# Kernel tuning notes

Measured on AMD Instinct MI355X. Metric: run time of the kernel, lower is better.

The kernel has to match this reference:

```python
import jax, jax.numpy as jnp
import numpy as np

EPS = 1e-5

def ln(x, g, b):
    m = x.mean(-1, keepdims=True)
    v = x.var(-1, keepdims=True)
    return (x - m) / jnp.sqrt(v + EPS) * g + b

def setup_inputs() -> dict:
    key = jax.random.key(0)
    ks = jax.random.split(key, 16)
    def p(k, shape, fan):
        return jax.random.normal(k, shape, jnp.float32) * (1.0 / np.sqrt(fan))
    B, N, M = 4, 256, 256
    C = 256
    inp = {}
    inp["tracks"] = jax.random.normal(ks[0], (B, 1028, N), jnp.float32)
    inp["detections"] = jax.random.normal(ks[1], (B, 1028, M), jnp.float32)
    # app encoder: Linear(1024,256) -> LN -> ReLU -> Linear(256,256)
    inp["wa1"] = p(ks[2], (1024, C), 1024); inp["ba1"] = jnp.zeros((C,), jnp.float32)
    inp["gla"] = jnp.ones((C,), jnp.float32); inp["bla"] = jnp.zeros((C,), jnp.float32)
    inp["wa2"] = p(ks[3], (C, C), C); inp["ba2"] = jnp.zeros((C,), jnp.float32)
    # geo encoder: Linear(4,128) -> LN -> ReLU -> Linear(128,256)
    inp["wg1"] = p(ks[4], (4, C // 2), 4); inp["bg1"] = jnp.zeros((C // 2,), jnp.float32)
    inp["glg"] = jnp.ones((C // 2,), jnp.float32); inp["blg"] = jnp.zeros((C // 2,), jnp.float32)
    inp["wg2"] = p(ks[5], (C // 2, C), C // 2); inp["bg2"] = jnp.zeros((C,), jnp.float32)
    # fusion LayerNorm
    inp["gf"] = jnp.ones((C,), jnp.float32); inp["bf"] = jnp.zeros((C,), jnp.float32)
    # cross-attention (4 heads, head_dim 64)
    inp["wq"] = p(ks[6], (C, C), C); inp["bq"] = jnp.zeros((C,), jnp.float32)
    inp["wk"] = p(ks[7], (C, C), C); inp["bk"] = jnp.zeros((C,), jnp.float32)
    inp["wv"] = p(ks[8], (C, C), C); inp["bv"] = jnp.zeros((C,), jnp.float32)
    inp["wo"] = p(ks[9], (C, C), C); inp["bo"] = jnp.zeros((C,), jnp.float32)
    # classifier: Linear(512,128) -> ReLU -> Linear(128,1)
    inp["wc1"] = p(ks[10], (2 * C, 128), 2 * C); inp["bc1"] = jnp.zeros((128,), jnp.float32)
    inp["wc2"] = p(ks[11], (128, 1), 128); inp["bc2"] = jnp.zeros((1,), jnp.float32)
    return inp

def reference(tracks, detections, wa1, ba1, gla, bla, wa2, ba2,
              wg1, bg1, glg, blg, wg2, bg2, gf, bf,
              wq, bq, wk, bk, wv, bv, wo, bo,
              wc1, bc1, wc2, bc2):
    tr = tracks.transpose(0, 2, 1)       # (B, N, 1028)
    de = detections.transpose(0, 2, 1)   # (B, M, 1028)

    def encode(x):
        app, geo = x[..., :1024], x[..., 1024:]
        h = jax.nn.relu(ln(app @ wa1 + ba1, gla, bla)) @ wa2 + ba2
        g = jax.nn.relu(ln(geo @ wg1 + bg1, glg, blg)) @ wg2 + bg2
        return ln(h + g, gf, bf)

    t_emb = encode(tr)   # (B, N, C)
    d_emb = encode(de)   # (B, M, C)

    B, N, C = t_emb.shape
    M = d_emb.shape[1]
    H, dh = 4, C // 4

    # Cross-attention (computed in the original forward but its output is never used)
    q = (t_emb @ wq + bq).reshape(B, N, H, dh)
    k = (d_emb @ wk + bk).reshape(B, M, H, dh)
    v = (d_emb @ wv + bv).reshape(B, M, H, dh)
    att = jax.nn.softmax(jnp.einsum('bnhd,bmhd->bhnm', q, k) / jnp.sqrt(jnp.float32(dh)), axis=-1)
    attn_out = jnp.einsum('bhnm,bmhd->bnhd', att, v).reshape(B, N, C) @ wo + bo  # unused, as in original

    # Pairwise classifier. cat([t_rep, d_rep], -1) @ wc1 == t @ wc1[:C] + d @ wc1[C:]
    a = t_emb @ wc1[:C]   # (B, N, 128)
    c = d_emb @ wc1[C:]   # (B, M, 128)
    h = jax.nn.relu(a[:, :, None, :] + c[:, None, :, :] + bc1)  # (B, N, M, 128)
    logits = (h @ wc2 + bc2)[..., 0]  # (B, N, M)
    return logits
```

## Files before the change

kernel.cpp:

```cpp
#include <hip/hip_runtime.h>

#define EPS 1e-5f


__global__ __launch_bounds__(256, 2) void k_gemm1(
    const float* __restrict__ tracks, const float* __restrict__ dets,
    const float* __restrict__ wa1, float* __restrict__ part)
{
    __shared__ __align__(16) float xs[128 * 32];
    const int blk = blockIdx.x;
    const int rt  = blk >> 3;
    const int ksi = blk & 7;
    const int g0  = rt * 32;
    const int side = g0 >> 10, b = (g0 >> 8) & 3, n0 = g0 & 255;
    const float* xb = (side ? dets : tracks) + (size_t)b * (1028 * 256);
    const int k0 = ksi * 128;
    const int tid = threadIdx.x;
    const int w   = tid >> 6;
    const int c0  = (tid & 63) * 4;

    for (int t = tid; t < 1024; t += 256) {
        int f = t >> 3, r4 = (t & 7) << 2;
        *(float4*)(xs + f * 32 + r4) =
            *(const float4*)(xb + (size_t)(k0 + f) * 256 + n0 + r4);
    }
    __syncthreads();

    float acc[8][4];
#pragma unroll
    for (int i = 0; i < 8; ++i)
#pragma unroll
        for (int j = 0; j < 4; ++j) acc[i][j] = 0.f;

    const float* wptr = wa1 + (size_t)k0 * 256 + c0;
    float4 wb[2][8];
#pragma unroll
    for (int j = 0; j < 8; ++j)
        wb[0][j] = *(const float4*)(wptr + (size_t)j * 256);

#pragma unroll
    for (int bb = 0; bb < 16; ++bb) {
        const int cur = bb & 1, nxt = cur ^ 1;
        if (bb < 15) {
#pragma unroll
            for (int j = 0; j < 8; ++j)
                wb[nxt][j] =
                    *(const float4*)(wptr + (size_t)((bb + 1) * 8 + j) * 256);
        }
#pragma unroll
        for (int j = 0; j < 8; ++j) {
            const int f = bb * 8 + j;
            float4 x0 = *(const float4*)(xs + f * 32 + w * 8);
            float4 x1 = *(const float4*)(xs + f * 32 + w * 8 + 4);
            float4 wv = wb[cur][j];
            float xv[8] = {x0.x, x0.y, x0.z, x0.w, x1.x, x1.y, x1.z, x1.w};
#pragma unroll
            for (int i = 0; i < 8; ++i) {
                acc[i][0] = fmaf(xv[i], wv.x, acc[i][0]);
                acc[i][1] = fmaf(xv[i], wv.y, acc[i][1]);
                acc[i][2] = fmaf(xv[i], wv.z, acc[i][2]);
                acc[i][3] = fmaf(xv[i], wv.w, acc[i][3]);
            }
        }
    }
    float* pb = part + ((size_t)ksi * 2048 + g0 + w * 8) * 256 + c0;
#pragma unroll
    for (int i = 0; i < 8; ++i)
        *(float4*)(pb + (size_t)i * 256) =
            make_float4(acc[i][0], acc[i][1], acc[i][2], acc[i][3]);
}

__global__ __launch_bounds__(256, 2) void k_tail(
    const float* __restrict__ tracks, const float* __restrict__ dets,
    const float* __restrict__ part,
    const float* __restrict__ ba1, const float* __restrict__ gla,
    const float* __restrict__ bla,
    const float* __restrict__ wg1, const float* __restrict__ bg1,
    const float* __restrict__ glg, const float* __restrict__ blg,
    const float* __restrict__ wa2, const float* __restrict__ ba2,
    const float* __restrict__ wg2, const float* __restrict__ bg2,
    const float* __restrict__ gf,  const float* __restrict__ bf,
    const float* __restrict__ wc1,
    float* __restrict__ aout, float* __restrict__ cout)
{
    __shared__ __align__(16) float h1e[384 * 4];
    __shared__ __align__(16) float psum[16 * 256];
    __shared__ __align__(16) float emb[256 * 4];
    __shared__ float ps2[2][4][128];
    __shared__ float red[4][4][2];
    __shared__ float geo_s[4][4];

    const int blk = blockIdx.x;
    const int g0 = blk * 4;
    const int side = g0 >> 10, b = (g0 >> 8) & 3, n0 = g0 & 255;
    const float* xb = (side ? dets : tracks) + (size_t)b * (1028 * 256);
    const int tid = threadIdx.x, w = tid >> 6, lane = tid & 63, c = tid;

    if (tid < 16)
        geo_s[tid >> 2][tid & 3] =
            xb[(size_t)(1024 + (tid & 3)) * 256 + n0 + (tid >> 2)];

    float h[4];
#pragma unroll
    for (int i = 0; i < 4; ++i) {
        float s = ba1[c];
#pragma unroll
        for (int s8 = 0; s8 < 8; ++s8)
            s += part[((size_t)s8 * 2048 + g0 + i) * 256 + c];
        h[i] = s;
    }
#pragma unroll
    for (int i = 0; i < 4; ++i) {
        float s = h[i], s2 = h[i] * h[i];
#pragma unroll
        for (int off = 32; off >= 1; off >>= 1) {
            s  += __shfl_xor(s,  off, 64);
            s2 += __shfl_xor(s2, off, 64);
        }
        if (lane == 0) { red[w][i][0] = s; red[w][i][1] = s2; }
    }
    __syncthreads();
    {
        float gv = gla[c], bv = bla[c];
#pragma unroll
        for (int i = 0; i < 4; ++i) {
            float s  = red[0][i][0] + red[1][i][0] + red[2][i][0] + red[3][i][0];
            float s2 = red[0][i][1] + red[1][i][1] + red[2][i][1] + red[3][i][1];
            float m   = s * (1.f / 256.f);
            float var = s2 * (1.f / 256.f) - m * m;
            h1e[c * 4 + i] =
                fmaxf((h[i] - m) * rsqrtf(var + EPS) * gv + bv, 0.f);
        }
    }
    __syncthreads();

    float gh[4];
    if (tid < 128) {
        const int j = tid;
#pragma unroll
        for (int i = 0; i < 4; ++i) {
            float s = bg1[j];
#pragma unroll
            for (int f = 0; f < 4; ++f)
                s = fmaf(geo_s[i][f], wg1[f * 128 + j], s);
            gh[i] = s;
        }
#pragma unroll
        for (int i = 0; i < 4; ++i) {
            float s = gh[i], s2 = gh[i] * gh[i];
#pragma unroll
            for (int off = 32; off >= 1; off >>= 1) {
                s  += __shfl_xor(s,  off, 64);
                s2 += __shfl_xor(s2, off, 64);
            }
            if (lane == 0) { red[w][i][0] = s; red[w][i][1] = s2; }
        }
    }
    __syncthreads();
    if (tid < 128) {
        const int j = tid;
        float gv = glg[j], bv = blg[j];
#pragma unroll
        for (int i = 0; i < 4; ++i) {
            float s  = red[0][i][0] + red[1][i][0];
            float s2 = red[0][i][1] + red[1][i][1];
            float m   = s * (1.f / 128.f);
            float var = s2 * (1.f / 128.f) - m * m;
            h1e[(256 + j) * 4 + i] =
                fmaxf((gh[i] - m) * rsqrtf(var + EPS) * gv + bv, 0.f);
        }
    }
    __syncthreads();

    const int c0 = lane * 4;
    float acc[4][4];
#pragma unroll
    for (int i = 0; i < 4; ++i)
#pragma unroll
        for (int j = 0; j < 4; ++j) acc[i][j] = 0.f;

    {
        const int ka = w * 64;
#pragma unroll 4
        for (int k = 0; k < 64; ++k) {
            float4 xv = *(const float4*)(h1e + (ka + k) * 4);
            float4 wv = *(const float4*)(wa2 + (size_t)(ka + k) * 256 + c0);
#pragma unroll
            for (int i = 0; i < 4; ++i) {
                float x = (&xv.x)[i];
                acc[i][0] = fmaf(x, wv.x, acc[i][0]);
                acc[i][1] = fmaf(x, wv.y, acc[i][1]);
                acc[i][2] = fmaf(x, wv.z, acc[i][2]);
                acc[i][3] = fmaf(x, wv.w, acc[i][3]);
            }
        }
        const int kg = w * 32;
#pragma unroll 4
        for (int k = 0; k < 32; ++k) {
            float4 xv = *(const float4*)(h1e + (256 + kg + k) * 4);
            float4 wv = *(const float4*)(wg2 + (size_t)(kg + k) * 256 + c0);
#pragma unroll
            for (int i = 0; i < 4; ++i) {
                float x = (&xv.x)[i];
                acc[i][0] = fmaf(x, wv.x, acc[i][0]);
                acc[i][1] = fmaf(x, wv.y, acc[i][1]);
                acc[i][2] = fmaf(x, wv.z, acc[i][2]);
                acc[i][3] = fmaf(x, wv.w, acc[i][3]);
            }
        }
    }
#pragma unroll
    for (int i = 0; i < 4; ++i)
        *(float4*)(psum + (w * 4 + i) * 256 + c0) =
            make_float4(acc[i][0], acc[i][1], acc[i][2], acc[i][3]);
    __syncthreads();

    float h2[4];
#pragma unroll
    for (int i = 0; i < 4; ++i) {
        float s = ba2[c] + bg2[c];
#pragma unroll
        for (int w4 = 0; w4 < 4; ++w4)
            s += psum[(w4 * 4 + i) * 256 + c];
        h2[i] = s;
    }
#pragma unroll
    for (int i = 0; i < 4; ++i) {
        float s = h2[i], s2 = h2[i] * h2[i];
#pragma unroll
        for (int off = 32; off >= 1; off >>= 1) {
            s  += __shfl_xor(s,  off, 64);
            s2 += __shfl_xor(s2, off, 64);
        }
        if (lane == 0) { red[w][i][0] = s; red[w][i][1] = s2; }
    }
    __syncthreads();
    {
        float gv = gf[c], bv = bf[c];
#pragma unroll
        for (int i = 0; i < 4; ++i) {
            float s  = red[0][i][0] + red[1][i][0] + red[2][i][0] + red[3][i][0];
            float s2 = red[0][i][1] + red[1][i][1] + red[2][i][1] + red[3][i][1];
            float m   = s * (1.f / 256.f);
            float var = s2 * (1.f / 256.f) - m * m;
            emb[c * 4 + i] = (h2[i] - m) * rsqrtf(var + EPS) * gv + bv;
        }
    }
    __syncthreads();

    const int half = tid >> 7, j = tid & 127;
    const float* wch = wc1 + (size_t)side * (256 * 128);
    float a4[4] = {0.f, 0.f, 0.f, 0.f};
#pragma unroll 4
    for (int k = 0; k < 128; ++k) {
        int kk = half * 128 + k;
        float wv = wch[(size_t)kk * 128 + j];
        float4 ev = *(const float4*)(emb + kk * 4);
        a4[0] = fmaf(ev.x, wv, a4[0]); a4[1] = fmaf(ev.y, wv, a4[1]);
        a4[2] = fmaf(ev.z, wv, a4[2]); a4[3] = fmaf(ev.w, wv, a4[3]);
    }
#pragma unroll
    for (int i = 0; i < 4; ++i) ps2[half][i][j] = a4[i];
    __syncthreads();

    float* outp = (side ? cout : aout) + ((size_t)b * 256 + n0) * 128;
    for (int idx = tid; idx < 512; idx += 256) {
        int i = idx >> 7, jo = idx & 127;
        outp[(size_t)i * 128 + jo] = ps2[0][i][jo] + ps2[1][i][jo];
    }
}

__global__ __launch_bounds__(256) void k_pairwise(
    const float* __restrict__ a, const float* __restrict__ cmat,
    const float* __restrict__ bc1, const float* __restrict__ wc2,
    const float* __restrict__ bc2, float* __restrict__ out)
{
    __shared__ float4 a_s[16 * 33];
    __shared__ float4 c_s[16 * 33];
    const int blk = blockIdx.x;
    const int b  = blk >> 8;
    const int n0 = ((blk >> 4) & 15) << 4;
    const int m0 = (blk & 15) << 4;
    const int tid = threadIdx.x;

    const float4* a4  = (const float4*)(a    + ((size_t)b * 256 + n0) * 128);
    const float4* c4  = (const float4*)(cmat + ((size_t)b * 256 + m0) * 128);
    const float4* b14 = (const float4*)bc1;
    for (int idx = tid; idx < 512; idx += 256) {
        int r = idx >> 5, q = idx & 31;
        float4 av = a4[r * 32 + q], bv = b14[q];
        a_s[r * 33 + q] = make_float4(av.x + bv.x, av.y + bv.y,
                                      av.z + bv.z, av.w + bv.w);
        c_s[r * 33 + q] = c4[r * 32 + q];
    }
    __syncthreads();

    const int ni = tid >> 4, mi = tid & 15;
    const float4* wp = (const float4*)wc2;
    float acc = bc2[0];
#pragma unroll 8
    for (int q = 0; q < 32; ++q) {
        float4 av = a_s[ni * 33 + q];
        float4 cv = c_s[mi * 33 + q];
        float4 wv = wp[q];
        acc = fmaf(fmaxf(av.x + cv.x, 0.f), wv.x, acc);
        acc = fmaf(fmaxf(av.y + cv.y, 0.f), wv.y, acc);
        acc = fmaf(fmaxf(av.z + cv.z, 0.f), wv.z, acc);
        acc = fmaf(fmaxf(av.w + cv.w, 0.f), wv.w, acc);
    }
    out[((size_t)b * 256 + n0 + ni) * 256 + m0 + mi] = acc;
}

extern "C" void kernel_launch(void* const* d_in, const int* in_sizes, int n_in,
                              void* d_out, int out_size, void* d_ws, size_t ws_size,
                              hipStream_t stream)
{
    const float* tracks = (const float*)d_in[0];
    const float* dets   = (const float*)d_in[1];
    const float* wa1 = (const float*)d_in[2];
    const float* ba1 = (const float*)d_in[3];
    const float* gla = (const float*)d_in[4];
    const float* bla = (const float*)d_in[5];
    const float* wa2 = (const float*)d_in[6];
    const float* ba2 = (const float*)d_in[7];
    const float* wg1 = (const float*)d_in[8];
    const float* bg1 = (const float*)d_in[9];
    const float* glg = (const float*)d_in[10];
    const float* blg = (const float*)d_in[11];
    const float* wg2 = (const float*)d_in[12];
    const float* bg2 = (const float*)d_in[13];
    const float* gf  = (const float*)d_in[14];
    const float* bf  = (const float*)d_in[15];
    const float* wc1 = (const float*)d_in[24];
    const float* bc1 = (const float*)d_in[25];
    const float* wc2 = (const float*)d_in[26];
    const float* bc2 = (const float*)d_in[27];
    float* out = (float*)d_out;
    float* ws  = (float*)d_ws;

    float* part = ws;
    float* aa   = ws + 4980736;
    float* cc   = ws + 5111808;

    hipLaunchKernelGGL(k_gemm1, dim3(512), dim3(256), 0, stream,
                       tracks, dets, wa1, part);
    hipLaunchKernelGGL(k_tail, dim3(512), dim3(256), 0, stream,
                       tracks, dets, part, ba1, gla, bla,
                       wg1, bg1, glg, blg, wa2, ba2, wg2, bg2,
                       gf, bf, wc1, aa, cc);
    hipLaunchKernelGGL(k_pairwise, dim3(1024), dim3(256), 0, stream,
                       aa, cc, bc1, wc2, bc2, out);
}
```

Before: 160.3 us.

## Fuse three kernels into one persistent kernel with software grid barriers

Merges the GEMM1, encoder-tail and pairwise kernels into a single 1024-block kernel separated by atomic-counter grid barriers, and re-tiles each phase so every block does half the previous per-block work (16-row GEMM tiles, 2-row tail). This removes two kernel launch gaps and lets all stages use the same grid. It relies on all 1024 blocks being co-resident (launch bounds of 4 blocks per SM) to avoid deadlock. The barrier adds spin-wait and fence costs, and the smaller tiles give less register-level reuse.

```diff
diff --git a/kernel.cpp b/kernel.cpp
--- a/kernel.cpp
+++ b/kernel.cpp
@@ -3,151 +3,141 @@
 #define EPS 1e-5f
 
 
-__global__ __launch_bounds__(256, 2) void k_gemm1(
-    const float* __restrict__ tracks, const float* __restrict__ dets,
-    const float* __restrict__ wa1, float* __restrict__ part)
+__device__ unsigned g_bar0, g_bar1;
+
+__device__ __forceinline__ void gbar(unsigned* ctr)
 {
-    __shared__ __align__(16) float xs[128 * 32];
-    const int blk = blockIdx.x;
-    const int rt  = blk >> 3;
-    const int ksi = blk & 7;
-    const int g0  = rt * 32;
-    const int side = g0 >> 10, b = (g0 >> 8) & 3, n0 = g0 & 255;
-    const float* xb = (side ? dets : tracks) + (size_t)b * (1028 * 256);
-    const int k0 = ksi * 128;
-    const int tid = threadIdx.x;
-    const int w   = tid >> 6;
-    const int c0  = (tid & 63) * 4;
-
-    for (int t = tid; t < 1024; t += 256) {
-        int f = t >> 3, r4 = (t & 7) << 2;
-        *(float4*)(xs + f * 32 + r4) =
-            *(const float4*)(xb + (size_t)(k0 + f) * 256 + n0 + r4);
+    __syncthreads();
+    __threadfence();
+    if (threadIdx.x == 0) {
+        unsigned ticket = atomicAdd(ctr, 1u);
+        unsigned target = (ticket & ~1023u) + 1024u;
+        while ((int)(__hip_atomic_load(ctr, __ATOMIC_RELAXED,
+                                       __HIP_MEMORY_SCOPE_AGENT) - target) < 0)
+            __builtin_amdgcn_s_sleep(2);
     }
     __syncthreads();
-
-    float acc[8][4];
-#pragma unroll
-    for (int i = 0; i < 8; ++i)
-#pragma unroll
-        for (int j = 0; j < 4; ++j) acc[i][j] = 0.f;
-
-    const float* wptr = wa1 + (size_t)k0 * 256 + c0;
-    float4 wb[2][8];
-#pragma unroll
-    for (int j = 0; j < 8; ++j)
-        wb[0][j] = *(const float4*)(wptr + (size_t)j * 256);
-
-#pragma unroll
-    for (int bb = 0; bb < 16; ++bb) {
-        const int cur = bb & 1, nxt = cur ^ 1;
-        if (bb < 15) {
-#pragma unroll
-            for (int j = 0; j < 8; ++j)
-                wb[nxt][j] =
-                    *(const float4*)(wptr + (size_t)((bb + 1) * 8 + j) * 256);
-        }
-#pragma unroll
-        for (int j = 0; j < 8; ++j) {
-            const int f = bb * 8 + j;
-            float4 x0 = *(const float4*)(xs + f * 32 + w * 8);
-            float4 x1 = *(const float4*)(xs + f * 32 + w * 8 + 4);
-            float4 wv = wb[cur][j];
-            float xv[8] = {x0.x, x0.y, x0.z, x0.w, x1.x, x1.y, x1.z, x1.w};
-#pragma unroll
-            for (int i = 0; i < 8; ++i) {
-                acc[i][0] = fmaf(xv[i], wv.x, acc[i][0]);
-                acc[i][1] = fmaf(xv[i], wv.y, acc[i][1]);
-                acc[i][2] = fmaf(xv[i], wv.z, acc[i][2]);
-                acc[i][3] = fmaf(xv[i], wv.w, acc[i][3]);
-            }
-        }
-    }
-    float* pb = part + ((size_t)ksi * 2048 + g0 + w * 8) * 256 + c0;
-#pragma unroll
-    for (int i = 0; i < 8; ++i)
-        *(float4*)(pb + (size_t)i * 256) =
-            make_float4(acc[i][0], acc[i][1], acc[i][2], acc[i][3]);
+    __threadfence();
 }
 
-__global__ __launch_bounds__(256, 2) void k_tail(
+__global__ __launch_bounds__(256, 4) void k_fused(
     const float* __restrict__ tracks, const float* __restrict__ dets,
-    const float* __restrict__ part,
-    const float* __restrict__ ba1, const float* __restrict__ gla,
-    const float* __restrict__ bla,
+    const float* __restrict__ wa1, const float* __restrict__ ba1,
+    const float* __restrict__ gla, const float* __restrict__ bla,
+    const float* __restrict__ wa2, const float* __restrict__ ba2,
     const float* __restrict__ wg1, const float* __restrict__ bg1,
     const float* __restrict__ glg, const float* __restrict__ blg,
-    const float* __restrict__ wa2, const float* __restrict__ ba2,
     const float* __restrict__ wg2, const float* __restrict__ bg2,
     const float* __restrict__ gf,  const float* __restrict__ bf,
-    const float* __restrict__ wc1,
-    float* __restrict__ aout, float* __restrict__ cout)
+    const float* __restrict__ wc1, const float* __restrict__ bc1,
+    const float* __restrict__ wc2, const float* __restrict__ bc2,
+    float* __restrict__ part, float* __restrict__ aa, float* __restrict__ cc,
+    float* __restrict__ out)
 {
-    __shared__ __align__(16) float h1e[384 * 4];
-    __shared__ __align__(16) float psum[16 * 256];
-    __shared__ __align__(16) float emb[256 * 4];
-    __shared__ float ps2[2][4][128];
-    __shared__ float red[4][4][2];
-    __shared__ float geo_s[4][4];
+    __shared__ __align__(16) float smem[4224];
+    __shared__ float red[4][2][2];
+    __shared__ float geo_s[2][4];
 
     const int blk = blockIdx.x;
-    const int g0 = blk * 4;
-    const int side = g0 >> 10, b = (g0 >> 8) & 3, n0 = g0 & 255;
-    const float* xb = (side ? dets : tracks) + (size_t)b * (1028 * 256);
-    const int tid = threadIdx.x, w = tid >> 6, lane = tid & 63, c = tid;
-
-    if (tid < 16)
-        geo_s[tid >> 2][tid & 3] =
-            xb[(size_t)(1024 + (tid & 3)) * 256 + n0 + (tid >> 2)];
-
-    float h[4];
-#pragma unroll
-    for (int i = 0; i < 4; ++i) {
-        float s = ba1[c];
-#pragma unroll
-        for (int s8 = 0; s8 < 8; ++s8)
-            s += part[((size_t)s8 * 2048 + g0 + i) * 256 + c];
-        h[i] = s;
+    const int tid = threadIdx.x;
+    const int w = tid >> 6, lane = tid & 63;
+
+    {
+        float* xs = smem;
+        const int rt  = blk >> 3;
+        const int ksi = blk & 7;
+        const int g0  = rt * 16;
+        const int side = g0 >> 10, b = (g0 >> 8) & 3, n0 = g0 & 255;
+        const float* xb = (side ? dets : tracks) + (size_t)b * (1028 * 256);
+        const int k0 = ksi * 128;
+        const int c0 = lane * 4;
+
+        for (int t = tid; t < 512; t += 256) {
+            int f = t >> 2, r4 = (t & 3) << 2;
+            *(float4*)(xs + f * 16 + r4) =
+                *(const float4*)(xb + (size_t)(k0 + f) * 256 + n0 + r4);
+        }
+        __syncthreads();
+
+        float acc[4][4];
+#pragma unroll
+        for (int i = 0; i < 4; ++i)
+#pragma unroll
+            for (int j = 0; j < 4; ++j) acc[i][j] = 0.f;
+
+        const float* wptr = wa1 + (size_t)k0 * 256 + c0;
+        float4 wb[2][4];
+#pragma unroll
+        for (int j = 0; j < 4; ++j)
+            wb[0][j] = *(const float4*)(wptr + (size_t)j * 256);
+
+#pragma unroll
+        for (int bb = 0; bb < 32; ++bb) {
+            const int cur = bb & 1, nxt = cur ^ 1;
+            if (bb < 31) {
+#pragma unroll
+                for (int j = 0; j < 4; ++j)
+                    wb[nxt][j] =
+                        *(const float4*)(wptr + (size_t)((bb + 1) * 4 + j) * 256);
+            }
+#pragma unroll
+            for (int j = 0; j < 4; ++j) {
+                const int f = bb * 4 + j;
+                float4 xv = *(const float4*)(xs + f * 16 + w * 4);
+                float4 wv = wb[cur][j];
+                acc[0][0] = fmaf(xv.x, wv.x, acc[0][0]);
+                acc[0][1] = fmaf(xv.x, wv.y, acc[0][1]);
+                acc[0][2] = fmaf(xv.x, wv.z, acc[0][2]);
+                acc[0][3] = fmaf(xv.x, wv.w, acc[0][3]);
+                acc[1][0] = fmaf(xv.y, wv.x, acc[1][0]);
+                acc[1][1] = fmaf(xv.y, wv.y, acc[1][1]);
+                acc[1][2] = fmaf(xv.y, wv.z, acc[1][2]);
+                acc[1][3] = fmaf(xv.y, wv.w, acc[1][3]);
+                acc[2][0] = fmaf(xv.z, wv.x, acc[2][0]);
+                acc[2][1] = fmaf(xv.z, wv.y, acc[2][1]);
+                acc[2][2] = fmaf(xv.z, wv.z, acc[2][2]);
+                acc[2][3] = fmaf(xv.z, wv.w, acc[2][3]);
+                acc[3][0] = fmaf(xv.w, wv.x, acc[3][0]);
+                acc[3][1] = fmaf(xv.w, wv.y, acc[3][1]);
+                acc[3][2] = fmaf(xv.w, wv.z, acc[3][2]);
+                acc[3][3] = fmaf(xv.w, wv.w, acc[3][3]);
+            }
+        }
+        float* pb = part + ((size_t)ksi * 2048 + g0 + w * 4) * 256 + c0;
+#pragma unroll
+        for (int i = 0; i < 4; ++i)
+            *(float4*)(pb + (size_t)i * 256) =
+                make_float4(acc[i][0], acc[i][1], acc[i][2], acc[i][3]);
     }
-#pragma unroll
-    for (int i = 0; i < 4; ++i) {
-        float s = h[i], s2 = h[i] * h[i];
-#pragma unroll
-        for (int off = 32; off >= 1; off >>= 1) {
-            s  += __shfl_xor(s,  off, 64);
-            s2 += __shfl_xor(s2, off, 64);
-        }
-        if (lane == 0) { red[w][i][0] = s; red[w][i][1] = s2; }
-    }
-    __syncthreads();
+
+    gbar(&g_bar0);
+
     {
-        float gv = gla[c], bv = bla[c];
-#pragma unroll
-        for (int i = 0; i < 4; ++i) {
-            float s  = red[0][i][0] + red[1][i][0] + red[2][i][0] + red[3][i][0];
-            float s2 = red[0][i][1] + red[1][i][1] + red[2][i][1] + red[3][i][1];
-            float m   = s * (1.f / 256.f);
-            float var = s2 * (1.f / 256.f) - m * m;
-            h1e[c * 4 + i] =
-                fmaxf((h[i] - m) * rsqrtf(var + EPS) * gv + bv, 0.f);
-        }
-    }
-    __syncthreads();
-
-    float gh[4];
-    if (tid < 128) {
-        const int j = tid;
-#pragma unroll
-        for (int i = 0; i < 4; ++i) {
-            float s = bg1[j];
-#pragma unroll
-            for (int f = 0; f < 4; ++f)
-                s = fmaf(geo_s[i][f], wg1[f * 128 + j], s);
-            gh[i] = s;
-        }
-#pragma unroll
-        for (int i = 0; i < 4; ++i) {
-            float s = gh[i], s2 = gh[i] * gh[i];
+        float* h1e  = smem;
+        float* psum = smem + 768;
+        float* emb  = smem + 2816;
+        float* ps2  = smem + 3328;
+        const int g0 = blk * 2;
+        const int side = g0 >> 10, b = (g0 >> 8) & 3, n0 = g0 & 255;
+        const float* xb = (side ? dets : tracks) + (size_t)b * (1028 * 256);
+        const int c = tid;
+
+        if (tid < 8)
+            geo_s[tid >> 2][tid & 3] =
+                xb[(size_t)(1024 + (tid & 3)) * 256 + n0 + (tid >> 2)];
+
+        float h[2];
+#pragma unroll
+        for (int i = 0; i < 2; ++i) {
+            float s = ba1[c];
+#pragma unroll
+            for (int s8 = 0; s8 < 8; ++s8)
+                s += part[((size_t)s8 * 2048 + g0 + i) * 256 + c];
+            h[i] = s;
+        }
+#pragma unroll
+        for (int i = 0; i < 2; ++i) {
+            float s = h[i], s2 = h[i] * h[i];
 #pragma unroll
             for (int off = 32; off >= 1; off >>= 1) {
                 s  += __shfl_xor(s,  off, 64);
@@ -155,160 +145,209 @@
             }
             if (lane == 0) { red[w][i][0] = s; red[w][i][1] = s2; }
         }
+        __syncthreads();
+        {
+            float gv = gla[c], bv = bla[c];
+            float o0, o1;
+            {
+                float s  = red[0][0][0] + red[1][0][0] + red[2][0][0] + red[3][0][0];
+                float s2 = red[0][0][1] + red[1][0][1] + red[2][0][1] + red[3][0][1];
+                float m = s * (1.f / 256.f), var = s2 * (1.f / 256.f) - m * m;
+                o0 = fmaxf((h[0] - m) * rsqrtf(var + EPS) * gv + bv, 0.f);
+            }
+            {
+                float s  = red[0][1][0] + red[1][1][0] + red[2][1][0] + red[3][1][0];
+                float s2 = red[0][1][1] + red[1][1][1] + red[2][1][1] + red[3][1][1];
+                float m = s * (1.f / 256.f), var = s2 * (1.f / 256.f) - m * m;
+                o1 = fmaxf((h[1] - m) * rsqrtf(var + EPS) * gv + bv, 0.f);
+            }
+            *(float2*)(h1e + c * 2) = make_float2(o0, o1);
+        }
+        __syncthreads();
+
+        float gh[2];
+        if (tid < 128) {
+            const int j = tid;
+#pragma unroll
+            for (int i = 0; i < 2; ++i) {
+                float s = bg1[j];
+#pragma unroll
+                for (int f = 0; f < 4; ++f)
+                    s = fmaf(geo_s[i][f], wg1[f * 128 + j], s);
+                gh[i] = s;
+            }
+#pragma unroll
+            for (int i = 0; i < 2; ++i) {
+                float s = gh[i], s2 = gh[i] * gh[i];
+#pragma unroll
+                for (int off = 32; off >= 1; off >>= 1) {
+                    s  += __shfl_xor(s,  off, 64);
+                    s2 += __shfl_xor(s2, off, 64);
+                }
+                if (lane == 0) { red[w][i][0] = s; red[w][i][1] = s2; }
+            }
+        }
+        __syncthreads();
+        if (tid < 128) {
+            const int j = tid;
+            float gv = glg[j], bv = blg[j];
+            float o0, o1;
+            {
+                float s  = red[0][0][0] + red[1][0][0];
+                float s2 = red[0][0][1] + red[1][0][1];
+                float m = s * (1.f / 128.f), var = s2 * (1.f / 128.f) - m * m;
+                o0 = fmaxf((gh[0] - m) * rsqrtf(var + EPS) * gv + bv, 0.f);
+            }
+            {
+                float s  = red[0][1][0] + red[1][1][0];
+                float s2 = red[0][1][1] + red[1][1][1];
+                float m = s * (1.f / 128.f), var = s2 * (1.f / 128.f) - m * m;
+                o1 = fmaxf((gh[1] - m) * rsqrtf(var + EPS) * gv + bv, 0.f);
+            }
+            *(float2*)(h1e + (256 + j) * 2) = make_float2(o0, o1);
+        }
+        __syncthreads();
+
+        const int c0 = lane * 4;
+        float acc[2][4];
+#pragma unroll
+        for (int i = 0; i < 2; ++i)
+#pragma unroll
+            for (int j = 0; j < 4; ++j) acc[i][j] = 0.f;
+        {
+            const int ka = w * 64;
+#pragma unroll 4
+            for (int k = 0; k < 64; ++k) {
+                float2 xv = *(const float2*)(h1e + (ka + k) * 2);
+                float4 wv = *(const float4*)(wa2 + (size_t)(ka + k) * 256 + c0);
+                acc[0][0] = fmaf(xv.x, wv.x, acc[0][0]);
+                acc[0][1] = fmaf(xv.x, wv.y, acc[0][1]);
+                acc[0][2] = fmaf(xv.x, wv.z, acc[0][2]);
+                acc[0][3] = fmaf(xv.x, wv.w, acc[0][3]);
+                acc[1][0] = fmaf(xv.y, wv.x, acc[1][0]);
+                acc[1][1] = fmaf(xv.y, wv.y, acc[1][1]);
+                acc[1][2] = fmaf(xv.y, wv.z, acc[1][2]);
+                acc[1][3] = fmaf(xv.y, wv.w, acc[1][3]);
+            }
+            const int kg = w * 32;
+#pragma unroll 4
+            for (int k = 0; k < 32; ++k) {
+                float2 xv = *(const float2*)(h1e + (256 + kg + k) * 2);
+                float4 wv = *(const float4*)(wg2 + (size_t)(kg + k) * 256 + c0);
+                acc[0][0] = fmaf(xv.x, wv.x, acc[0][0]);
+                acc[0][1] = fmaf(xv.x, wv.y, acc[0][1]);
+                acc[0][2] = fmaf(xv.x, wv.z, acc[0][2]);
+                acc[0][3] = fmaf(xv.x, wv.w, acc[0][3]);
+                acc[1][0] = fmaf(xv.y, wv.x, acc[1][0]);
+                acc[1][1] = fmaf(xv.y, wv.y, acc[1][1]);
+                acc[1][2] = fmaf(xv.y, wv.z, acc[1][2]);
+                acc[1][3] = fmaf(xv.y, wv.w, acc[1][3]);
+            }
+        }
+#pragma unroll
+        for (int i = 0; i < 2; ++i)
+            *(float4*)(psum + (w * 2 + i) * 256 + c0) =
+                make_float4(acc[i][0], acc[i][1], acc[i][2], acc[i][3]);
+        __syncthreads();
+
+        float h2[2];
+#pragma unroll
+        for (int i = 0; i < 2; ++i) {
+            float s = ba2[c] + bg2[c];
+#pragma unroll
+            for (int w4 = 0; w4 < 4; ++w4)
+                s += psum[(w4 * 2 + i) * 256 + c];
+            h2[i] = s;
+        }
+#pragma unroll
+        for (int i = 0; i < 2; ++i) {
+            float s = h2[i], s2 = h2[i] * h2[i];
+#pragma unroll
+            for (int off = 32; off >= 1; off >>= 1) {
+                s  += __shfl_xor(s,  off, 64);
+                s2 += __shfl_xor(s2, off, 64);
+            }
+            if (lane == 0) { red[w][i][0] = s; red[w][i][1] = s2; }
+        }
+        __syncthreads();
+        {
+            float gv = gf[c], bv = bf[c];
+            float e0, e1;
+            {
+                float s  = red[0][0][0] + red[1][0][0] + red[2][0][0] + red[3][0][0];
+                float s2 = red[0][0][1] + red[1][0][1] + red[2][0][1] + red[3][0][1];
+                float m = s * (1.f / 256.f), var = s2 * (1.f / 256.f) - m * m;
+                e0 = (h2[0] - m) * rsqrtf(var + EPS) * gv + bv;
+            }
+            {
+                float s  = red[0][1][0] + red[1][1][0] + red[2][1][0] + red[3][1][0];
+                float s2 = red[0][1][1] + red[1][1][1] + red[2][1][1] + red[3][1][1];
+                float m = s * (1.f / 256.f), var = s2 * (1.f / 256.f) - m * m;
+                e1 = (h2[1] - m) * rsqrtf(var + EPS) * gv + bv;
+            }
+            *(float2*)(emb + c * 2) = make_float2(e0, e1);
+        }
+        __syncthreads();
+
+        const int half = tid >> 7, j = tid & 127;
+        const float* wch = wc1 + (size_t)side * (256 * 128);
+        float p0 = 0.f, p1 = 0.f;
+#pragma unroll 4
+        for (int k = 0; k < 128; ++k) {
+            int kk = half * 128 + k;
+            float wv = wch[(size_t)kk * 128 + j];
+            float2 ev = *(const float2*)(emb + kk * 2);
+            p0 = fmaf(ev.x, wv, p0);
+            p1 = fmaf(ev.y, wv, p1);
+        }
+        ps2[(half * 2 + 0) * 128 + j] = p0;
+        ps2[(half * 2 + 1) * 128 + j] = p1;
+        __syncthreads();
+
+        float* outp = (side ? cc : aa) + ((size_t)b * 256 + n0) * 128;
+        {
+            int i = tid >> 7, jo = tid & 127;
+            outp[(size_t)i * 128 + jo] =
+                ps2[i * 128 + jo] + ps2[(2 + i) * 128 + jo];
+        }
     }
-    __syncthreads();
-    if (tid < 128) {
-        const int j = tid;
-        float gv = glg[j], bv = blg[j];
-#pragma unroll
-        for (int i = 0; i < 4; ++i) {
-            float s  = red[0][i][0] + red[1][i][0];
-            float s2 = red[0][i][1] + red[1][i][1];
-            float m   = s * (1.f / 128.f);
-            float var = s2 * (1.f / 128.f) - m * m;
-            h1e[(256 + j) * 4 + i] =
-                fmaxf((gh[i] - m) * rsqrtf(var + EPS) * gv + bv, 0.f);
-        }
+
+    gbar(&g_bar1);
+
+    {
+        float4* a_s = (float4*)smem;
+        float4* c_s = ((float4*)smem) + 528;
+        const int b  = blk >> 8;
+        const int n0 = ((blk >> 4) & 15) << 4;
+        const int m0 = (blk & 15) << 4;
+
+        const float4* a4  = (const float4*)(aa + ((size_t)b * 256 + n0) * 128);
+        const float4* c4  = (const float4*)(cc + ((size_t)b * 256 + m0) * 128);
+        const float4* b14 = (const float4*)bc1;
+        for (int idx = tid; idx < 512; idx += 256) {
+            int r = idx >> 5, q = idx & 31;
+            float4 av = a4[r * 32 + q], bv = b14[q];
+            a_s[r * 33 + q] = make_float4(av.x + bv.x, av.y + bv.y,
+                                          av.z + bv.z, av.w + bv.w);
+            c_s[r * 33 + q] = c4[r * 32 + q];
+        }
+        __syncthreads();
+
+        const int ni = tid >> 4, mi = tid & 15;
+        const float4* wp = (const float4*)wc2;
+        float acc = bc2[0];
+#pragma unroll 8
+        for (int q = 0; q < 32; ++q) {
+            float4 av = a_s[ni * 33 + q];
+            float4 cv = c_s[mi * 33 + q];
+            float4 wv = wp[q];
+            acc = fmaf(fmaxf(av.x + cv.x, 0.f), wv.x, acc);
+            acc = fmaf(fmaxf(av.y + cv.y, 0.f), wv.y, acc);
+            acc = fmaf(fmaxf(av.z + cv.z, 0.f), wv.z, acc);
+            acc = fmaf(fmaxf(av.w + cv.w, 0.f), wv.w, acc);
+        }
+        out[((size_t)b * 256 + n0 + ni) * 256 + m0 + mi] = acc;
     }
-    __syncthreads();
-
-    const int c0 = lane * 4;
-    float acc[4][4];
-#pragma unroll
-    for (int i = 0; i < 4; ++i)
-#pragma unroll
-        for (int j = 0; j < 4; ++j) acc[i][j] = 0.f;
-
-    {
-        const int ka = w * 64;
-#pragma unroll 4
-        for (int k = 0; k < 64; ++k) {
-            float4 xv = *(const float4*)(h1e + (ka + k) * 4);
-            float4 wv = *(const float4*)(wa2 + (size_t)(ka + k) * 256 + c0);
-#pragma unroll
-            for (int i = 0; i < 4; ++i) {
-                float x = (&xv.x)[i];
-                acc[i][0] = fmaf(x, wv.x, acc[i][0]);
-                acc[i][1] = fmaf(x, wv.y, acc[i][1]);
-                acc[i][2] = fmaf(x, wv.z, acc[i][2]);
-                acc[i][3] = fmaf(x, wv.w, acc[i][3]);
-            }
-        }
-        const int kg = w * 32;
-#pragma unroll 4
-        for (int k = 0; k < 32; ++k) {
-            float4 xv = *(const float4*)(h1e + (256 + kg + k) * 4);
-            float4 wv = *(const float4*)(wg2 + (size_t)(kg + k) * 256 + c0);
-#pragma unroll
-            for (int i = 0; i < 4; ++i) {
-                float x = (&xv.x)[i];
-                acc[i][0] = fmaf(x, wv.x, acc[i][0]);
-                acc[i][1] = fmaf(x, wv.y, acc[i][1]);
-                acc[i][2] = fmaf(x, wv.z, acc[i][2]);
-                acc[i][3] = fmaf(x, wv.w, acc[i][3]);
-            }
-        }
-    }
-#pragma unroll
-    for (int i = 0; i < 4; ++i)
-        *(float4*)(psum + (w * 4 + i) * 256 + c0) =
-            make_float4(acc[i][0], acc[i][1], acc[i][2], acc[i][3]);
-    __syncthreads();
-
-    float h2[4];
-#pragma unroll
-    for (int i = 0; i < 4; ++i) {
-        float s = ba2[c] + bg2[c];
-#pragma unroll
-        for (int w4 = 0; w4 < 4; ++w4)
-            s += psum[(w4 * 4 + i) * 256 + c];
-        h2[i] = s;
-    }
-#pragma unroll
-    for (int i = 0; i < 4; ++i) {
-        float s = h2[i], s2 = h2[i] * h2[i];
-#pragma unroll
-        for (int off = 32; off >= 1; off >>= 1) {
-            s  += __shfl_xor(s,  off, 64);
-            s2 += __shfl_xor(s2, off, 64);
-        }
-        if (lane == 0) { red[w][i][0] = s; red[w][i][1] = s2; }
-    }
-    __syncthreads();
-    {
-        float gv = gf[c], bv = bf[c];
-#pragma unroll
-        for (int i = 0; i < 4; ++i) {
-            float s  = red[0][i][0] + red[1][i][0] + red[2][i][0] + red[3][i][0];
-            float s2 = red[0][i][1] + red[1][i][1] + red[2][i][1] + red[3][i][1];
-            float m   = s * (1.f / 256.f);
-            float var = s2 * (1.f / 256.f) - m * m;
-            emb[c * 4 + i] = (h2[i] - m) * rsqrtf(var + EPS) * gv + bv;
-        }
-    }
-    __syncthreads();
-
-    const int half = tid >> 7, j = tid & 127;
-    const float* wch = wc1 + (size_t)side * (256 * 128);
-    float a4[4] = {0.f, 0.f, 0.f, 0.f};
-#pragma unroll 4
-    for (int k = 0; k < 128; ++k) {
-        int kk = half * 128 + k;
-        float wv = wch[(size_t)kk * 128 + j];
-        float4 ev = *(const float4*)(emb + kk * 4);
-        a4[0] = fmaf(ev.x, wv, a4[0]); a4[1] = fmaf(ev.y, wv, a4[1]);
-        a4[2] = fmaf(ev.z, wv, a4[2]); a4[3] = fmaf(ev.w, wv, a4[3]);
-    }
-#pragma unroll
-    for (int i = 0; i < 4; ++i) ps2[half][i][j] = a4[i];
-    __syncthreads();
-
-    float* outp = (side ? cout : aout) + ((size_t)b * 256 + n0) * 128;
-    for (int idx = tid; idx < 512; idx += 256) {
-        int i = idx >> 7, jo = idx & 127;
-        outp[(size_t)i * 128 + jo] = ps2[0][i][jo] + ps2[1][i][jo];
-    }
-}
-
-__global__ __launch_bounds__(256) void k_pairwise(
-    const float* __restrict__ a, const float* __restrict__ cmat,
-    const float* __restrict__ bc1, const float* __restrict__ wc2,
-    const float* __restrict__ bc2, float* __restrict__ out)
-{
-    __shared__ float4 a_s[16 * 33];
-    __shared__ float4 c_s[16 * 33];
-    const int blk = blockIdx.x;
-    const int b  = blk >> 8;
-    const int n0 = ((blk >> 4) & 15) << 4;
-    const int m0 = (blk & 15) << 4;
-    const int tid = threadIdx.x;
-
-    const float4* a4  = (const float4*)(a    + ((size_t)b * 256 + n0) * 128);
-    const float4* c4  = (const float4*)(cmat + ((size_t)b * 256 + m0) * 128);
-    const float4* b14 = (const float4*)bc1;
-    for (int idx = tid; idx < 512; idx += 256) {
-        int r = idx >> 5, q = idx & 31;
-        float4 av = a4[r * 32 + q], bv = b14[q];
-        a_s[r * 33 + q] = make_float4(av.x + bv.x, av.y + bv.y,
-                                      av.z + bv.z, av.w + bv.w);
-        c_s[r * 33 + q] = c4[r * 32 + q];
-    }
-    __syncthreads();
-
-    const int ni = tid >> 4, mi = tid & 15;
-    const float4* wp = (const float4*)wc2;
-    float acc = bc2[0];
-#pragma unroll 8
-    for (int q = 0; q < 32; ++q) {
-        float4 av = a_s[ni * 33 + q];
-        float4 cv = c_s[mi * 33 + q];
-        float4 wv = wp[q];
-        acc = fmaf(fmaxf(av.x + cv.x, 0.f), wv.x, acc);
-        acc = fmaf(fmaxf(av.y + cv.y, 0.f), wv.y, acc);
-        acc = fmaf(fmaxf(av.z + cv.z, 0.f), wv.z, acc);
-        acc = fmaf(fmaxf(av.w + cv.w, 0.f), wv.w, acc);
-    }
-    out[((size_t)b * 256 + n0 + ni) * 256 + m0 + mi] = acc;
 }
 
 extern "C" void kernel_launch(void* const* d_in, const int* in_sizes, int n_in,
@@ -342,12 +381,8 @@
     float* aa   = ws + 4980736;
     float* cc   = ws + 5111808;
 
-    hipLaunchKernelGGL(k_gemm1, dim3(512), dim3(256), 0, stream,
-                       tracks, dets, wa1, part);
-    hipLaunchKernelGGL(k_tail, dim3(512), dim3(256), 0, stream,
-                       tracks, dets, part, ba1, gla, bla,
-                       wg1, bg1, glg, blg, wa2, ba2, wg2, bg2,
-                       gf, bf, wc1, aa, cc);
-    hipLaunchKernelGGL(k_pairwise, dim3(1024), dim3(256), 0, stream,
-                       aa, cc, bc1, wc2, bc2, out);
+    hipLaunchKernelGGL(k_fused, dim3(1024), dim3(256), 0, stream,
+                       tracks, dets, wa1, ba1, gla, bla, wa2, ba2,
+                       wg1, bg1, glg, blg, wg2, bg2, gf, bf,
+                       wc1, bc1, wc2, bc2, part, aa, cc, out);
 }
```

Result: slower. 620.0 us (+286.8%).
